# Kernel optimization log

Measured on AMD Instinct MI355X. Metric: run time of the kernel, lower is better.

## Reference

```python
import jax, jax.numpy as jnp
import numpy as np

B, H, T, D = 2, 16, 2048, 64


def setup_inputs() -> dict:
    key = jax.random.key(0)
    kq, kk, kv = jax.random.split(key, 3)
    Q = jax.random.normal(kq, (B, H, T, D), dtype=jnp.float32)
    K = jax.random.normal(kk, (B, H, T, D), dtype=jnp.float32)
    V = jax.random.normal(kv, (B, H, T, D), dtype=jnp.float32)
    return {"Q": Q, "K": K, "V": V}


def reference(Q, K, V):
    # Q,K,V: [B,H,T,D]; causal self-attention with 1/sqrt(D) temperature.
    Bq, Hq, Tq, Dq = Q.shape
    temperature = jnp.asarray(Dq, Q.dtype) ** 0.5
    # [B,H,T,T] attention scores
    scores = jnp.einsum('bhqd,bhkd->bhqk', Q, K) / temperature
    causal = jnp.tril(jnp.ones((Tq, Tq), dtype=bool))  # [T,T]
    scores = jnp.where(causal[None, None, :, :], scores, jnp.finfo(Q.dtype).min)
    weights = jax.nn.softmax(scores, axis=-1)
    return jnp.einsum('bhqk,bhkd->bhqd', weights, V)
```

## Files before the change

### kernel.cpp

```cpp
#include <hip/hip_runtime.h>
#include <hip/hip_bf16.h>
#include <math.h>


#define BATCH 2
#define HEADS 16
#define SEQ   2048
#define DIM   64
#define NBH   (BATCH * HEADS)
#define NKT_G (SEQ / 64)
#define TILE_SHORTS 4096

typedef __attribute__((ext_vector_type(8)))  short    bf16x8;
typedef __attribute__((ext_vector_type(4)))  unsigned u32x4;
typedef __attribute__((ext_vector_type(4)))  float    f32x4;
typedef __attribute__((ext_vector_type(16))) float    f32x16;

__device__ inline short f2bf(float f) {
    unsigned u = __builtin_bit_cast(unsigned, f);
    u += 0x7fff + ((u >> 16) & 1);
    return (short)(u >> 16);
}

__device__ inline unsigned cvtpk(float a, float b) {
    unsigned r;
    asm("v_cvt_pk_bf16_f32 %0, %1, %2" : "=v"(r) : "v"(a), "v"(b));
    return r;
}

__global__ __launch_bounds__(256)
void prep_kv(const float* __restrict__ K, const float* __restrict__ V,
             short* __restrict__ Kimg, short* __restrict__ Vimg) {
    const int tile = blockIdx.x;
    const int tid  = threadIdx.x;
    const float* Ksrc = K + (size_t)tile * TILE_SHORTS;
    const float* Vsrc = V + (size_t)tile * TILE_SHORTS;
    char* Kdst = (char*)(Kimg + (size_t)tile * TILE_SHORTS);
    char* Vdst = (char*)(Vimg + (size_t)tile * TILE_SHORTS);

    __shared__ float vt[64][65];

    {
        const int r  = tid >> 2;
        const int c0 = (tid & 3) * 16;
        #pragma unroll
        for (int j = 0; j < 16; j += 4) {
            const f32x4 v = *reinterpret_cast<const f32x4*>(Vsrc + (size_t)r * 64 + c0 + j);
            vt[r][c0+j] = v[0]; vt[r][c0+j+1] = v[1]; vt[r][c0+j+2] = v[2]; vt[r][c0+j+3] = v[3];
        }
    }

    const int f = tid >> 6;
    const int l = tid & 63;
    const int l31 = l & 31;
    const int l8  = (l >> 5) * 8;

    #pragma unroll
    for (int kb = 0; kb < 2; ++kb) {
        const float* src = Ksrc + (size_t)(kb * 32 + l31) * 64 + f * 16 + l8;
        const f32x4 a = *reinterpret_cast<const f32x4*>(src);
        const f32x4 b = *reinterpret_cast<const f32x4*>(src + 4);
        short h[8];
        #pragma unroll
        for (int j = 0; j < 4; ++j) { h[j] = f2bf(a[j]); h[4+j] = f2bf(b[j]); }
        *reinterpret_cast<bf16x8*>(Kdst + ((kb * 4 + f) * 64 + l) * 16) =
            *reinterpret_cast<bf16x8*>(h);
    }

    __syncthreads();

    #pragma unroll
    for (int db = 0; db < 2; ++db) {
        const int d  = db * 32 + l31;
        const int k0 = f * 16 + l8;
        short h[8];
        #pragma unroll
        for (int j = 0; j < 8; ++j) h[j] = f2bf(vt[k0 + j][d]);
        *reinterpret_cast<bf16x8*>(Vdst + ((db * 4 + f) * 64 + l) * 16) =
            *reinterpret_cast<bf16x8*>(h);
    }
}

__global__ __launch_bounds__(128)
void fa_fwd(const float* __restrict__ Q, const short* __restrict__ Kimg,
            const short* __restrict__ Vimg, float* __restrict__ O) {
    const int tid  = threadIdx.x;
    const int lane = tid & 63;
    const int wid  = tid >> 6;
    const int q31  = lane & 31;
    const int hi2  = lane >> 5;

    const int idx = blockIdx.x;
    const int bh  = idx & 31;
    const int j   = idx >> 5;
    const int k8  = j >> 3;
    const int g8  = j & 7;
    const int p   = (k8 & 1) ? (k8 * 8 + 7 - g8) : j;
    const int qw  = p * 32;
    const int kd  = p >> 1;
    const int qrel = (p & 1) * 32 + q31;

    const float* Qb = Q + (size_t)bh * SEQ * DIM;
    float*       Ob = O + (size_t)bh * SEQ * DIM;
    const char*  Ktb = (const char*)(Kimg + (size_t)bh * NKT_G * TILE_SHORTS);
    const char*  Vtb = (const char*)(Vimg + (size_t)bh * NKT_G * TILE_SHORTS);
    const unsigned lb = (unsigned)lane * 16;

    __shared__ float accL[32][64];
    __shared__ float rsL[32];

    const float SCL = 0.18033688011112042f;
    bf16x8 qf[4];
    #pragma unroll
    for (int ds = 0; ds < 4; ++ds) {
        const float* src = Qb + (size_t)(qw + q31) * DIM + ds * 16 + hi2 * 8;
        const f32x4 a = *reinterpret_cast<const f32x4*>(src);
        const f32x4 b = *reinterpret_cast<const f32x4*>(src + 4);
        bf16x8 q;
        #pragma unroll
        for (int jj = 0; jj < 4; ++jj) {
            q[jj]     = f2bf(a[jj] * SCL);
            q[4 + jj] = f2bf(b[jj] * SCL);
        }
        qf[ds] = q;
    }

    f32x16 acc0 = {}, acc1 = {};
    float rs = 0.f;

    for (int kt = wid; kt <= kd; kt += 2) {
        const char* Kt = Ktb + (size_t)kt * 8192;
        const char* Vt = Vtb + (size_t)kt * 8192;

        bf16x8 kf[2][4], vf[2][4];
        #pragma unroll
        for (int kb = 0; kb < 2; ++kb)
            #pragma unroll
            for (int ds = 0; ds < 4; ++ds)
                kf[kb][ds] = *reinterpret_cast<const bf16x8*>(
                    Kt + (kb * 4 + ds) * 1024 + lb);
        #pragma unroll
        for (int db = 0; db < 2; ++db)
            #pragma unroll
            for (int s = 0; s < 4; ++s)
                vf[db][s] = *reinterpret_cast<const bf16x8*>(
                    Vt + (db * 4 + s) * 1024 + lb);

        f32x16 st0 = {}, st1 = {};
        __builtin_amdgcn_s_setprio(1);
        #pragma unroll
        for (int ds = 0; ds < 4; ++ds)
            st0 = __builtin_amdgcn_mfma_f32_32x32x16_bf16(kf[0][ds], qf[ds], st0, 0, 0, 0);
        #pragma unroll
        for (int ds = 0; ds < 4; ++ds)
            st1 = __builtin_amdgcn_mfma_f32_32x32x16_bf16(kf[1][ds], qf[ds], st1, 0, 0, 0);
        __builtin_amdgcn_s_setprio(0);

        const bool lastt = (kt == kd);
        float p0[16], p1[16];
        #pragma unroll
        for (int r = 0; r < 16; ++r) {
            const int kloc = (r & 3) + 8 * (r >> 2) + 4 * hi2;
            float v0 = __builtin_amdgcn_exp2f(st0[r]);
            float v1 = __builtin_amdgcn_exp2f(st1[r]);
            if (lastt) {
                if (kloc > qrel)      v0 = 0.f;
                if (kloc + 32 > qrel) v1 = 0.f;
            }
            p0[r] = v0; p1[r] = v1;
            rs += v0 + v1;
        }

        __builtin_amdgcn_s_setprio(1);
        #pragma unroll
        for (int s = 0; s < 4; ++s) {
            const float* pk = (s >> 1) ? p1 : p0;
            const int u = (s & 1) * 8;
            unsigned Xa = cvtpk(pk[u],     pk[u + 1]);
            unsigned Ya = cvtpk(pk[u + 2], pk[u + 3]);
            unsigned Xb = cvtpk(pk[u + 4], pk[u + 5]);
            unsigned Yb = cvtpk(pk[u + 6], pk[u + 7]);
            asm("v_permlane32_swap_b32 %0, %1" : "+v"(Xa), "+v"(Xb));
            asm("v_permlane32_swap_b32 %0, %1" : "+v"(Ya), "+v"(Yb));
            const u32x4 w = {Xa, Ya, Xb, Yb};
            const bf16x8 pa = __builtin_bit_cast(bf16x8, w);
            acc0 = __builtin_amdgcn_mfma_f32_32x32x16_bf16(pa, vf[0][s], acc0, 0, 0, 0);
            acc1 = __builtin_amdgcn_mfma_f32_32x32x16_bf16(pa, vf[1][s], acc1, 0, 0, 0);
        }
        __builtin_amdgcn_s_setprio(0);
    }

    rs += __shfl_xor(rs, 32, 64);

    if (wid == 0) {
        #pragma unroll
        for (int r = 0; r < 16; ++r) {
            const int off = (r & 3) + 8 * (r >> 2) + 4 * hi2;
            accL[off][q31]      = acc0[r];
            accL[off][q31 + 32] = acc1[r];
        }
        if (lane < 32) rsL[lane] = rs;
    }
    __syncthreads();

    if (wid == 1) {
        const float rstot = rs + rsL[q31];
        const float inv = 1.0f / rstot;
        #pragma unroll
        for (int r = 0; r < 16; ++r) {
            const int off = (r & 3) + 8 * (r >> 2) + 4 * hi2;
            const float ir = __shfl(inv, off, 64);
            const float o0 = acc0[r] + accL[off][q31];
            const float o1 = acc1[r] + accL[off][q31 + 32];
            float* dst = Ob + (size_t)(qw + off) * DIM + q31;
            dst[0]  = o0 * ir;
            dst[32] = o1 * ir;
        }
    }
}

extern "C" void kernel_launch(void* const* d_in, const int* in_sizes, int n_in,
                              void* d_out, int out_size, void* d_ws, size_t ws_size,
                              hipStream_t stream) {
    const float* Q = (const float*)d_in[0];
    const float* K = (const float*)d_in[1];
    const float* V = (const float*)d_in[2];
    float*       O = (float*)d_out;

    short* Kimg = (short*)d_ws;
    short* Vimg = (short*)d_ws + (size_t)NBH * NKT_G * TILE_SHORTS;

    prep_kv<<<dim3(NBH * NKT_G), dim3(256), 0, stream>>>(K, V, Kimg, Vimg);
    fa_fwd<<<dim3(NBH * 64), dim3(128), 0, stream>>>(Q, Kimg, Vimg, O);
}
```

Baseline: 49.04 us.

## Pair causal q-tiles per block, split keys across four waves, prefetch K

Each block now handles two mirrored 32-row query tiles (p and 63-p) one after the other, which balances causal work across blocks and halves the grid. Four waves instead of two split the key tiles, and their partial accumulators and row sums are reduced through larger shared-memory buffers. K fragments for the next tile are double-buffered in registers so their load overlaps the current tile's compute. The cost is higher register pressure, an extra barrier per half, and fewer blocks in flight.

```diff
diff --git a/kernel.cpp b/kernel.cpp
--- a/kernel.cpp
+++ b/kernel.cpp
@@ -81,24 +81,18 @@
     }
 }
 
-__global__ __launch_bounds__(128)
+__global__ __launch_bounds__(256)
 void fa_fwd(const float* __restrict__ Q, const short* __restrict__ Kimg,
             const short* __restrict__ Vimg, float* __restrict__ O) {
     const int tid  = threadIdx.x;
     const int lane = tid & 63;
-    const int wid  = tid >> 6;
+    const int w    = tid >> 6;
     const int q31  = lane & 31;
     const int hi2  = lane >> 5;
 
     const int idx = blockIdx.x;
     const int bh  = idx & 31;
-    const int j   = idx >> 5;
-    const int k8  = j >> 3;
-    const int g8  = j & 7;
-    const int p   = (k8 & 1) ? (k8 * 8 + 7 - g8) : j;
-    const int qw  = p * 32;
-    const int kd  = p >> 1;
-    const int qrel = (p & 1) * 32 + q31;
+    const int jp  = idx >> 5;
 
     const float* Qb = Q + (size_t)bh * SEQ * DIM;
     float*       Ob = O + (size_t)bh * SEQ * DIM;
@@ -106,116 +100,149 @@
     const char*  Vtb = (const char*)(Vimg + (size_t)bh * NKT_G * TILE_SHORTS);
     const unsigned lb = (unsigned)lane * 16;
 
-    __shared__ float accL[32][64];
-    __shared__ float rsL[32];
+    __shared__ float accL[3][32][64];
+    __shared__ float rsL[3][32];
 
     const float SCL = 0.18033688011112042f;
-    bf16x8 qf[4];
-    #pragma unroll
-    for (int ds = 0; ds < 4; ++ds) {
-        const float* src = Qb + (size_t)(qw + q31) * DIM + ds * 16 + hi2 * 8;
-        const f32x4 a = *reinterpret_cast<const f32x4*>(src);
-        const f32x4 b = *reinterpret_cast<const f32x4*>(src + 4);
-        bf16x8 q;
-        #pragma unroll
-        for (int jj = 0; jj < 4; ++jj) {
-            q[jj]     = f2bf(a[jj] * SCL);
-            q[4 + jj] = f2bf(b[jj] * SCL);
-        }
-        qf[ds] = q;
-    }
-
-    f32x16 acc0 = {}, acc1 = {};
-    float rs = 0.f;
-
-    for (int kt = wid; kt <= kd; kt += 2) {
-        const char* Kt = Ktb + (size_t)kt * 8192;
-        const char* Vt = Vtb + (size_t)kt * 8192;
-
-        bf16x8 kf[2][4], vf[2][4];
-        #pragma unroll
-        for (int kb = 0; kb < 2; ++kb)
+
+    #pragma unroll 1
+    for (int half = 0; half < 2; ++half) {
+        const int p    = half ? (63 - jp) : jp;
+        const int kdc  = p >> 1;
+        const int qrel = (p & 1) * 32 + q31;
+        const int qw   = p * 32;
+
+        bf16x8 qf[4];
+        #pragma unroll
+        for (int ds = 0; ds < 4; ++ds) {
+            const float* src = Qb + (size_t)(qw + q31) * DIM + ds * 16 + hi2 * 8;
+            const f32x4 a = *reinterpret_cast<const f32x4*>(src);
+            const f32x4 b = *reinterpret_cast<const f32x4*>(src + 4);
+            bf16x8 q;
+            #pragma unroll
+            for (int jj = 0; jj < 4; ++jj) {
+                q[jj]     = f2bf(a[jj] * SCL);
+                q[4 + jj] = f2bf(b[jj] * SCL);
+            }
+            qf[ds] = q;
+        }
+
+        f32x16 acc0 = {}, acc1 = {};
+        float rs = 0.f;
+
+        bf16x8 kfA[2][4], kfB[2][4];
+
+        auto loadK = [&](bf16x8 (&kf)[2][4], int kt) {
+            const char* Kt = Ktb + (size_t)kt * 8192;
+            #pragma unroll
+            for (int kb = 0; kb < 2; ++kb)
+                #pragma unroll
+                for (int ds = 0; ds < 4; ++ds)
+                    kf[kb][ds] = *reinterpret_cast<const bf16x8*>(
+                        Kt + (kb * 4 + ds) * 1024 + lb);
+        };
+
+        auto compute = [&](bf16x8 (&kf)[2][4], int kt) {
+            const char* Vt = Vtb + (size_t)kt * 8192;
+            bf16x8 vf[2][4];
+            #pragma unroll
+            for (int db = 0; db < 2; ++db)
+                #pragma unroll
+                for (int s = 0; s < 4; ++s)
+                    vf[db][s] = *reinterpret_cast<const bf16x8*>(
+                        Vt + (db * 4 + s) * 1024 + lb);
+
+            f32x16 st0 = {}, st1 = {};
+            __builtin_amdgcn_s_setprio(1);
             #pragma unroll
             for (int ds = 0; ds < 4; ++ds)
-                kf[kb][ds] = *reinterpret_cast<const bf16x8*>(
-                    Kt + (kb * 4 + ds) * 1024 + lb);
-        #pragma unroll
-        for (int db = 0; db < 2; ++db)
-            #pragma unroll
-            for (int s = 0; s < 4; ++s)
-                vf[db][s] = *reinterpret_cast<const bf16x8*>(
-                    Vt + (db * 4 + s) * 1024 + lb);
-
-        f32x16 st0 = {}, st1 = {};
-        __builtin_amdgcn_s_setprio(1);
-        #pragma unroll
-        for (int ds = 0; ds < 4; ++ds)
-            st0 = __builtin_amdgcn_mfma_f32_32x32x16_bf16(kf[0][ds], qf[ds], st0, 0, 0, 0);
-        #pragma unroll
-        for (int ds = 0; ds < 4; ++ds)
-            st1 = __builtin_amdgcn_mfma_f32_32x32x16_bf16(kf[1][ds], qf[ds], st1, 0, 0, 0);
-        __builtin_amdgcn_s_setprio(0);
-
-        const bool lastt = (kt == kd);
-        float p0[16], p1[16];
-        #pragma unroll
-        for (int r = 0; r < 16; ++r) {
-            const int kloc = (r & 3) + 8 * (r >> 2) + 4 * hi2;
-            float v0 = __builtin_amdgcn_exp2f(st0[r]);
-            float v1 = __builtin_amdgcn_exp2f(st1[r]);
-            if (lastt) {
-                if (kloc > qrel)      v0 = 0.f;
-                if (kloc + 32 > qrel) v1 = 0.f;
-            }
-            p0[r] = v0; p1[r] = v1;
-            rs += v0 + v1;
-        }
-
-        __builtin_amdgcn_s_setprio(1);
-        #pragma unroll
-        for (int s = 0; s < 4; ++s) {
-            const float* pk = (s >> 1) ? p1 : p0;
-            const int u = (s & 1) * 8;
-            unsigned Xa = cvtpk(pk[u],     pk[u + 1]);
-            unsigned Ya = cvtpk(pk[u + 2], pk[u + 3]);
-            unsigned Xb = cvtpk(pk[u + 4], pk[u + 5]);
-            unsigned Yb = cvtpk(pk[u + 6], pk[u + 7]);
-            asm("v_permlane32_swap_b32 %0, %1" : "+v"(Xa), "+v"(Xb));
-            asm("v_permlane32_swap_b32 %0, %1" : "+v"(Ya), "+v"(Yb));
-            const u32x4 w = {Xa, Ya, Xb, Yb};
-            const bf16x8 pa = __builtin_bit_cast(bf16x8, w);
-            acc0 = __builtin_amdgcn_mfma_f32_32x32x16_bf16(pa, vf[0][s], acc0, 0, 0, 0);
-            acc1 = __builtin_amdgcn_mfma_f32_32x32x16_bf16(pa, vf[1][s], acc1, 0, 0, 0);
-        }
-        __builtin_amdgcn_s_setprio(0);
-    }
-
-    rs += __shfl_xor(rs, 32, 64);
-
-    if (wid == 0) {
-        #pragma unroll
-        for (int r = 0; r < 16; ++r) {
-            const int off = (r & 3) + 8 * (r >> 2) + 4 * hi2;
-            accL[off][q31]      = acc0[r];
-            accL[off][q31 + 32] = acc1[r];
-        }
-        if (lane < 32) rsL[lane] = rs;
-    }
-    __syncthreads();
-
-    if (wid == 1) {
-        const float rstot = rs + rsL[q31];
-        const float inv = 1.0f / rstot;
-        #pragma unroll
-        for (int r = 0; r < 16; ++r) {
-            const int off = (r & 3) + 8 * (r >> 2) + 4 * hi2;
-            const float ir = __shfl(inv, off, 64);
-            const float o0 = acc0[r] + accL[off][q31];
-            const float o1 = acc1[r] + accL[off][q31 + 32];
-            float* dst = Ob + (size_t)(qw + off) * DIM + q31;
-            dst[0]  = o0 * ir;
-            dst[32] = o1 * ir;
-        }
+                st0 = __builtin_amdgcn_mfma_f32_32x32x16_bf16(kf[0][ds], qf[ds], st0, 0, 0, 0);
+            #pragma unroll
+            for (int ds = 0; ds < 4; ++ds)
+                st1 = __builtin_amdgcn_mfma_f32_32x32x16_bf16(kf[1][ds], qf[ds], st1, 0, 0, 0);
+            __builtin_amdgcn_s_setprio(0);
+
+            const bool lastt = (kt == kdc);
+            float p0[16], p1[16];
+            #pragma unroll
+            for (int r = 0; r < 16; ++r) {
+                const int kloc = (r & 3) + 8 * (r >> 2) + 4 * hi2;
+                float v0 = __builtin_amdgcn_exp2f(st0[r]);
+                float v1 = __builtin_amdgcn_exp2f(st1[r]);
+                if (lastt) {
+                    if (kloc > qrel)      v0 = 0.f;
+                    if (kloc + 32 > qrel) v1 = 0.f;
+                }
+                p0[r] = v0; p1[r] = v1;
+                rs += v0 + v1;
+            }
+
+            __builtin_amdgcn_s_setprio(1);
+            #pragma unroll
+            for (int s = 0; s < 4; ++s) {
+                const float* pk = (s >> 1) ? p1 : p0;
+                const int u = (s & 1) * 8;
+                unsigned Xa = cvtpk(pk[u],     pk[u + 1]);
+                unsigned Ya = cvtpk(pk[u + 2], pk[u + 3]);
+                unsigned Xb = cvtpk(pk[u + 4], pk[u + 5]);
+                unsigned Yb = cvtpk(pk[u + 6], pk[u + 7]);
+                asm("v_permlane32_swap_b32 %0, %1" : "+v"(Xa), "+v"(Xb));
+                asm("v_permlane32_swap_b32 %0, %1" : "+v"(Ya), "+v"(Yb));
+                const u32x4 ww = {Xa, Ya, Xb, Yb};
+                const bf16x8 pa = __builtin_bit_cast(bf16x8, ww);
+                acc0 = __builtin_amdgcn_mfma_f32_32x32x16_bf16(pa, vf[0][s], acc0, 0, 0, 0);
+                acc1 = __builtin_amdgcn_mfma_f32_32x32x16_bf16(pa, vf[1][s], acc1, 0, 0, 0);
+            }
+            __builtin_amdgcn_s_setprio(0);
+        };
+
+        int kt = w;
+        if (kt <= kdc) {
+            loadK(kfA, kt);
+            while (true) {
+                int ktn = kt + 4;
+                const bool vB = (ktn <= kdc);
+                if (vB) loadK(kfB, ktn);
+                compute(kfA, kt);
+                if (!vB) break;
+                kt = ktn; ktn = kt + 4;
+                const bool vA = (ktn <= kdc);
+                if (vA) loadK(kfA, ktn);
+                compute(kfB, kt);
+                if (!vA) break;
+                kt = ktn;
+            }
+        }
+
+        rs += __shfl_xor(rs, 32, 64);
+
+        if (w > 0) {
+            #pragma unroll
+            for (int r = 0; r < 16; ++r) {
+                const int off = (r & 3) + 8 * (r >> 2) + 4 * hi2;
+                accL[w - 1][off][q31]      = acc0[r];
+                accL[w - 1][off][q31 + 32] = acc1[r];
+            }
+            if (lane < 32) rsL[w - 1][lane] = rs;
+        }
+        __syncthreads();
+        if (w == 0) {
+            const float rstot = rs + rsL[0][q31] + rsL[1][q31] + rsL[2][q31];
+            const float inv = 1.0f / rstot;
+            #pragma unroll
+            for (int r = 0; r < 16; ++r) {
+                const int off = (r & 3) + 8 * (r >> 2) + 4 * hi2;
+                const float ir = __shfl(inv, off, 64);
+                const float o0 = acc0[r] + accL[0][off][q31]
+                               + accL[1][off][q31] + accL[2][off][q31];
+                const float o1 = acc1[r] + accL[0][off][q31 + 32]
+                               + accL[1][off][q31 + 32] + accL[2][off][q31 + 32];
+                float* dst = Ob + (size_t)(qw + off) * DIM + q31;
+                dst[0]  = o0 * ir;
+                dst[32] = o1 * ir;
+            }
+        }
+        __syncthreads();
     }
 }
 
@@ -231,5 +258,5 @@
     short* Vimg = (short*)d_ws + (size_t)NBH * NKT_G * TILE_SHORTS;
 
     prep_kv<<<dim3(NBH * NKT_G), dim3(256), 0, stream>>>(K, V, Kimg, Vimg);
-    fa_fwd<<<dim3(NBH * 64), dim3(128), 0, stream>>>(Q, Kimg, Vimg, O);
-}
+    fa_fwd<<<dim3(NBH * 32), dim3(256), 0, stream>>>(Q, Kimg, Vimg, O);
+}
```

Result: slower. 67.45 us (+37.5%).
